# Performance work log

Hardware: AMD Instinct MI355X
Metric: run time of the kernel (lower is better)

The kernel has to match this reference:

```python
import jax, jax.numpy as jnp
import numpy as np

N_NODES = 100000
N_EDGES = 1600000
D = 128
NUM_EXPERTS = 8
NUM_LAYERS = 2
EPS = 1e-5


def setup_inputs() -> dict:
    key = jax.random.key(0)
    ks = jax.random.split(key, 8)
    x = jax.random.normal(ks[0], (N_NODES, D), dtype=jnp.float32)
    edge_index = jax.random.randint(ks[1], (2, N_EDGES), 0, N_NODES, dtype=jnp.int64)
    # weights scaled for sane numerics (like torch default inits)
    W_self = jax.random.normal(ks[2], (NUM_EXPERTS, NUM_LAYERS, D, D), dtype=jnp.float32) * 0.05
    W_nbr = jax.random.normal(ks[3], (NUM_EXPERTS, NUM_LAYERS, D, D), dtype=jnp.float32) * 0.05
    b = jax.random.normal(ks[4], (NUM_EXPERTS, NUM_LAYERS, D), dtype=jnp.float32) * 0.05
    gamma = jnp.ones((NUM_EXPERTS, NUM_LAYERS - 1, D), dtype=jnp.float32)
    beta = jnp.zeros((NUM_EXPERTS, NUM_LAYERS - 1, D), dtype=jnp.float32)
    return {"x": x, "edge_index": edge_index, "W_self": W_self, "W_nbr": W_nbr,
            "b": b, "gamma": gamma, "beta": beta}


def _sage_encoder(x, src, dst, inv_deg, W_self, W_nbr, b, gamma, beta):
    # One GraphSAGE-style encoder: per layer, mean-aggregate neighbor feats,
    # transform self + neighbor, then BatchNorm + ReLU (all but last layer).
    h = x
    for l in range(NUM_LAYERS):
        agg = jax.ops.segment_sum(h[src], dst, num_segments=N_NODES) * inv_deg  # [N, d]
        h = h @ W_self[l] + agg @ W_nbr[l] + b[l]
        if l < NUM_LAYERS - 1:
            mean = jnp.mean(h, axis=0)
            var = jnp.var(h, axis=0)
            h = gamma[l] * (h - mean) * jax.lax.rsqrt(var + EPS) + beta[l]
            h = jax.nn.relu(h)
        # dropout: identity in inference mode
    return h  # [N, d]


def reference(x, edge_index, W_self, W_nbr, b, gamma, beta):
    src, dst = edge_index[0], edge_index[1]
    deg = jax.ops.segment_sum(jnp.ones((N_EDGES,), x.dtype), dst, num_segments=N_NODES)
    inv_deg = (1.0 / jnp.maximum(deg, 1.0))[:, None]  # [N, 1]
    outs = [
        _sage_encoder(x, src, dst, inv_deg, W_self[e], W_nbr[e], b[e], gamma[e], beta[e])
        for e in range(NUM_EXPERTS)
    ]
    return jnp.stack(outs, axis=-1)  # [N, hidden, num_experts]
```

## Files before the change

### kernel.cpp

```cpp
#include <hip/hip_runtime.h>
#include <stdint.h>

#define NN 100000
#define NED 1600000
#define DD 128
#define NE 8
#define ND ((size_t)NN * (size_t)DD)
#define NDE (ND * NE)
#define BNEPS 1e-5f

typedef __attribute__((ext_vector_type(8))) short short8;
typedef __attribute__((ext_vector_type(4))) float float4v;
typedef __attribute__((ext_vector_type(4))) unsigned int uint4v;

__device__ __forceinline__ float bf2f(uint32_t h) {
    union { uint32_t u; float f; } c; c.u = h << 16; return c.f;
}
__device__ __forceinline__ uint16_t f2bf(float x) {
    union { float f; uint32_t u; } c; c.f = x;
    uint32_t r = (c.u + 0x7fffu + ((c.u >> 16) & 1u)) >> 16;
    return (uint16_t)r;
}

__global__ __launch_bounds__(256) void k_deg(const int* __restrict__ dst, int* __restrict__ deg) {
    int i = blockIdx.x * 256 + threadIdx.x;
    int stride = gridDim.x * 256;
    for (; i < NED; i += stride) atomicAdd(&deg[dst[i]], 1);
}

__global__ __launch_bounds__(1024) void k_scan1(const int* __restrict__ deg, int* __restrict__ rp,
                                                int* __restrict__ bsum) {
    __shared__ int sh[1024];
    int t = threadIdx.x;
    int i = blockIdx.x * 1024 + t;
    int v = (i < NN) ? deg[i] : 0;
    sh[t] = v; __syncthreads();
    for (int off = 1; off < 1024; off <<= 1) {
        int add = (t >= off) ? sh[t - off] : 0;
        __syncthreads();
        sh[t] += add;
        __syncthreads();
    }
    if (i < NN) rp[i] = sh[t] - v;
    if (t == 1023) bsum[blockIdx.x] = sh[1023];
}

__global__ void k_scan2(int* bsum) {
    if (threadIdx.x == 0) {
        int acc = 0;
        for (int j = 0; j < 98; ++j) { int t = bsum[j]; bsum[j] = acc; acc += t; }
    }
}

__global__ __launch_bounds__(1024) void k_scan3(const int* __restrict__ deg, int* __restrict__ rp,
                                                const int* __restrict__ bsum, int* __restrict__ cur,
                                                float* __restrict__ invd) {
    int i = blockIdx.x * 1024 + threadIdx.x;
    if (i == 0) rp[NN] = NED;
    if (i < NN) {
        int r = rp[i] + bsum[blockIdx.x];
        rp[i] = r; cur[i] = r;
        invd[i] = 1.0f / fmaxf((float)deg[i], 1.0f);
    }
}

__global__ __launch_bounds__(256) void k_scatter(const int* __restrict__ src, const int* __restrict__ dst,
                                                 int* __restrict__ cur, int* __restrict__ esrc) {
    int i = blockIdx.x * 256 + threadIdx.x;
    int stride = gridDim.x * 256;
    for (; i < NED; i += stride) {
        int d = dst[i];
        int p = atomicAdd(&cur[d], 1);
        esrc[p] = src[i];
    }
}

__global__ __launch_bounds__(256) void k_castx(const float* __restrict__ x, uint16_t* __restrict__ xb) {
    size_t i = ((size_t)blockIdx.x * 256 + threadIdx.x) * 8;
    if (i >= ND) return;
    float4 a = *(const float4*)(x + i);
    float4 b = *(const float4*)(x + i + 4);
    uint4 u;
    u.x = (uint32_t)f2bf(a.x) | ((uint32_t)f2bf(a.y) << 16);
    u.y = (uint32_t)f2bf(a.z) | ((uint32_t)f2bf(a.w) << 16);
    u.z = (uint32_t)f2bf(b.x) | ((uint32_t)f2bf(b.y) << 16);
    u.w = (uint32_t)f2bf(b.z) | ((uint32_t)f2bf(b.w) << 16);
    *(uint4*)(xb + i) = u;
}

__global__ __launch_bounds__(256) void k_agg(const uint16_t* __restrict__ sp, uint16_t* __restrict__ dp,
                                             const int* __restrict__ rp, const int* __restrict__ esrc,
                                             const float* __restrict__ invd) {
    int wave = threadIdx.x >> 6, lane = threadIdx.x & 63;
    int node = blockIdx.x * 4 + wave;
    if (node >= NN) return;
    int beg = rp[node], end = rp[node + 1];
    float s0 = 0, s1 = 0, t0 = 0, t1 = 0, u0 = 0, u1 = 0, w0 = 0, w1 = 0;
    int i = beg;
    for (; i + 3 < end; i += 4) {
        int a = esrc[i], b = esrc[i + 1], c = esrc[i + 2], d = esrc[i + 3];
        uint32_t va = *(const uint32_t*)(sp + (size_t)a * DD + lane * 2);
        uint32_t vb = *(const uint32_t*)(sp + (size_t)b * DD + lane * 2);
        uint32_t vc = *(const uint32_t*)(sp + (size_t)c * DD + lane * 2);
        uint32_t vd = *(const uint32_t*)(sp + (size_t)d * DD + lane * 2);
        s0 += bf2f(va & 0xffff); s1 += bf2f(va >> 16);
        t0 += bf2f(vb & 0xffff); t1 += bf2f(vb >> 16);
        u0 += bf2f(vc & 0xffff); u1 += bf2f(vc >> 16);
        w0 += bf2f(vd & 0xffff); w1 += bf2f(vd >> 16);
    }
    for (; i < end; ++i) {
        uint32_t va = *(const uint32_t*)(sp + (size_t)esrc[i] * DD + lane * 2);
        s0 += bf2f(va & 0xffff); s1 += bf2f(va >> 16);
    }
    float id = invd[node];
    s0 = (s0 + t0 + u0 + w0) * id; s1 = (s1 + t1 + u1 + w1) * id;
    *(uint32_t*)(dp + (size_t)node * DD + lane * 2) = (uint32_t)f2bf(s0) | ((uint32_t)f2bf(s1) << 16);
}

__device__ __forceinline__ void acc_u4(float* a, uint4 u) {
    a[0] += bf2f(u.x & 0xffffu); a[1] += bf2f(u.x >> 16);
    a[2] += bf2f(u.y & 0xffffu); a[3] += bf2f(u.y >> 16);
    a[4] += bf2f(u.z & 0xffffu); a[5] += bf2f(u.z >> 16);
    a[6] += bf2f(u.w & 0xffffu); a[7] += bf2f(u.w >> 16);
}

__global__ __launch_bounds__(256) void k_agg8(const uint16_t* __restrict__ Hi,
                                              uint16_t* __restrict__ A2i,
                                              const int* __restrict__ rp,
                                              const int* __restrict__ esrc,
                                              const float* __restrict__ invd) {
    int wave = threadIdx.x >> 6, lane = threadIdx.x & 63;
    int node = blockIdx.x * 4 + wave;
    if (node >= NN) return;
    int beg = rp[node], end = rp[node + 1];
    float acc[16];
#pragma unroll
    for (int j = 0; j < 16; ++j) acc[j] = 0.f;
    const size_t loff = (size_t)(lane * 16);
    int i = beg;
    for (; i + 3 < end; i += 4) {
        const uint16_t* p0 = Hi + (size_t)esrc[i] * 1024 + loff;
        const uint16_t* p1 = Hi + (size_t)esrc[i + 1] * 1024 + loff;
        const uint16_t* p2 = Hi + (size_t)esrc[i + 2] * 1024 + loff;
        const uint16_t* p3 = Hi + (size_t)esrc[i + 3] * 1024 + loff;
        uint4 a0 = *(const uint4*)p0;
        uint4 a1 = *(const uint4*)(p0 + 8);
        uint4 b0 = *(const uint4*)p1;
        uint4 b1 = *(const uint4*)(p1 + 8);
        uint4 c0 = *(const uint4*)p2;
        uint4 c1 = *(const uint4*)(p2 + 8);
        uint4 d0 = *(const uint4*)p3;
        uint4 d1 = *(const uint4*)(p3 + 8);
        acc_u4(acc, a0); acc_u4(acc + 8, a1);
        acc_u4(acc, b0); acc_u4(acc + 8, b1);
        acc_u4(acc, c0); acc_u4(acc + 8, c1);
        acc_u4(acc, d0); acc_u4(acc + 8, d1);
    }
    for (; i < end; ++i) {
        const uint16_t* pa = Hi + (size_t)esrc[i] * 1024 + loff;
        uint4 a0 = *(const uint4*)pa;
        uint4 a1 = *(const uint4*)(pa + 8);
        acc_u4(acc, a0); acc_u4(acc + 8, a1);
    }
    float id = invd[node];
    uint32_t pk[8];
#pragma unroll
    for (int j = 0; j < 8; ++j)
        pk[j] = (uint32_t)f2bf(acc[2 * j] * id) | ((uint32_t)f2bf(acc[2 * j + 1] * id) << 16);
    uint4v o0 = {pk[0], pk[1], pk[2], pk[3]};
    uint4v o1 = {pk[4], pk[5], pk[6], pk[7]};
    uint16_t* dp = A2i + (size_t)node * 1024 + loff;
    __builtin_nontemporal_store(o0, (uint4v*)dp);
    __builtin_nontemporal_store(o1, (uint4v*)(dp + 8));
}

__global__ __launch_bounds__(256, 2) void k_gemm(
    const float* __restrict__ Wself, const float* __restrict__ Wnbr, const float* __restrict__ bglob,
    int layer,
    const uint16_t* __restrict__ A1, const uint16_t* __restrict__ A2, int a_rstride, int a_ezoff,
    uint16_t* __restrict__ outb, int out_mode, float* __restrict__ outf,
    int do_stats, float* __restrict__ stats) {
    __shared__ __align__(16) uint16_t wlds[128 * 256];
    __shared__ float ssum[128];
    __shared__ float ssq[128];
    int tid = threadIdx.x;
    int e = blockIdx.z;
    size_t wbase = ((size_t)e * 2 + layer) * (128 * 128);

    for (int i = tid; i < 128 * 32; i += 256) {
        int n = i & 127, g = i >> 7;
        uint16_t tmp[8];
#pragma unroll
        for (int j = 0; j < 8; ++j) {
            int k = g * 8 + j;
            float w = (k < 128) ? Wself[wbase + (size_t)k * 128 + n]
                                : Wnbr[wbase + (size_t)(k - 128) * 128 + n];
            tmp[j] = f2bf(w);
        }
        uint4 u;
        u.x = (uint32_t)tmp[0] | ((uint32_t)tmp[1] << 16);
        u.y = (uint32_t)tmp[2] | ((uint32_t)tmp[3] << 16);
        u.z = (uint32_t)tmp[4] | ((uint32_t)tmp[5] << 16);
        u.w = (uint32_t)tmp[6] | ((uint32_t)tmp[7] << 16);
        *(uint4*)&wlds[n * 256 + (((g ^ n) & 31) << 3)] = u;
    }
    if (tid < 128) { ssum[tid] = 0.f; ssq[tid] = 0.f; }
    __syncthreads();

    const uint16_t* A1p = A1 + (size_t)e * a_ezoff;
    const uint16_t* A2p = A2 + (size_t)e * a_ezoff;

    int wave = tid >> 6, lane = tid & 63;
    int m = lane & 15, quad = lane >> 4;
    int rowBase = blockIdx.x * 256 + wave * 64;

    float4v acc[4][8];
#pragma unroll
    for (int rt = 0; rt < 4; ++rt)
#pragma unroll
        for (int nt = 0; nt < 8; ++nt)
            acc[rt][nt] = (float4v){0.f, 0.f, 0.f, 0.f};

#pragma unroll
    for (int ks = 0; ks < 8; ++ks) {
        int kk = ks * 32 + quad * 8;
        short8 af[4];
#pragma unroll
        for (int rt = 0; rt < 4; ++rt) {
            int row = rowBase + rt * 16 + m;
            row = row < NN ? row : NN - 1;
            const uint16_t* ap = (kk < 128) ? (A1p + (size_t)row * a_rstride + kk)
                                            : (A2p + (size_t)row * a_rstride + (kk - 128));
            af[rt] = *(const short8*)ap;
        }
        int g = kk >> 3;
#pragma unroll
        for (int nt = 0; nt < 8; ++nt) {
            int n = nt * 16 + m;
            short8 bf = *(const short8*)&wlds[n * 256 + (((g ^ n) & 31) << 3)];
#pragma unroll
            for (int rt = 0; rt < 4; ++rt)
                acc[rt][nt] = __builtin_amdgcn_mfma_f32_16x16x32_bf16(af[rt], bf, acc[rt][nt], 0, 0, 0);
        }
    }

    float csum[8], csq[8];
#pragma unroll
    for (int nt = 0; nt < 8; ++nt) { csum[nt] = 0.f; csq[nt] = 0.f; }

    size_t bofs = ((size_t)e * 2 + layer) * 128;
#pragma unroll
    for (int rt = 0; rt < 4; ++rt) {
#pragma unroll
        for (int nt = 0; nt < 8; ++nt) {
            int col = nt * 16 + m;
            float bv = bglob[bofs + col];
#pragma unroll
            for (int r = 0; r < 4; ++r) {
                int row = rowBase + rt * 16 + quad * 4 + r;
                if (row < NN) {
                    float v = acc[rt][nt][r] + bv;
                    if (out_mode == 0) outb[(size_t)row * 1024 + (size_t)e * 128 + col] = f2bf(v);
                    else if (out_mode == 1) outb[(size_t)e * ND + (size_t)row * DD + col] = f2bf(v);
                    else outf[(size_t)row * 1024 + col * 8 + e] = v;
                    if (do_stats) { csum[nt] += v; csq[nt] += v * v; }
                }
            }
        }
    }

    if (do_stats) {
#pragma unroll
        for (int nt = 0; nt < 8; ++nt) {
            float s = csum[nt], q = csq[nt];
            s += __shfl_xor(s, 16); q += __shfl_xor(q, 16);
            s += __shfl_xor(s, 32); q += __shfl_xor(q, 32);
            if (quad == 0) {
                atomicAdd(&ssum[nt * 16 + m], s);
                atomicAdd(&ssq[nt * 16 + m], q);
            }
        }
        __syncthreads();
        if (tid < 128) {
            atomicAdd(&stats[e * 256 + tid], ssum[tid]);
            atomicAdd(&stats[e * 256 + 128 + tid], ssq[tid]);
        }
    }
}

__global__ void k_coef(const float* __restrict__ stats, const float* __restrict__ gamma,
                       const float* __restrict__ beta, float* __restrict__ coef) {
    int e = blockIdx.x;
    int f = threadIdx.x;
    float s = stats[e * 256 + f], ss = stats[e * 256 + 128 + f];
    float mean = s / (float)NN;
    float var = ss / (float)NN - mean * mean;
    float sc = gamma[e * 128 + f] * rsqrtf(var + BNEPS);
    coef[e * 256 + f] = sc;
    coef[e * 256 + 128 + f] = beta[e * 128 + f] - mean * sc;
}

__global__ __launch_bounds__(256) void k_affine(uint16_t* __restrict__ H, const float* __restrict__ coef) {
    size_t i = ((size_t)blockIdx.x * 256 + threadIdx.x) * 8;
    if (i >= NDE) return;
    int e = (int)((i >> 7) & 7);
    int ff = (int)(i & 127);
    const float* sc = coef + e * 256;
    const float* sf = sc + 128;
    uint4 u = *(const uint4*)(H + i);
    uint32_t w[4] = {u.x, u.y, u.z, u.w};
    uint32_t o[4];
#pragma unroll
    for (int j = 0; j < 4; ++j) {
        float v0 = fmaxf(bf2f(w[j] & 0xffffu) * sc[ff + 2 * j] + sf[ff + 2 * j], 0.f);
        float v1 = fmaxf(bf2f(w[j] >> 16) * sc[ff + 2 * j + 1] + sf[ff + 2 * j + 1], 0.f);
        o[j] = (uint32_t)f2bf(v0) | ((uint32_t)f2bf(v1) << 16);
    }
    uint4 ou = {o[0], o[1], o[2], o[3]};
    *(uint4*)(H + i) = ou;
}

__global__ __launch_bounds__(256) void k_transpose(const uint16_t* __restrict__ O, float* __restrict__ out) {
    size_t t = (size_t)blockIdx.x * 256 + threadIdx.x;
    if (t >= ND / 2) return;
    size_t idx = t * 2;
    float v0[8], v1[8];
#pragma unroll
    for (int e = 0; e < 8; ++e) {
        uint32_t u = *(const uint32_t*)(O + (size_t)e * ND + idx);
        v0[e] = bf2f(u & 0xffff); v1[e] = bf2f(u >> 16);
    }
    float* op = out + idx * 8;
    float4 a = {v0[0], v0[1], v0[2], v0[3]}, b = {v0[4], v0[5], v0[6], v0[7]};
    float4 c = {v1[0], v1[1], v1[2], v1[3]}, d = {v1[4], v1[5], v1[6], v1[7]};
    *(float4*)(op) = a; *(float4*)(op + 4) = b; *(float4*)(op + 8) = c; *(float4*)(op + 12) = d;
}

extern "C" void kernel_launch(void* const* d_in, const int* in_sizes, int n_in,
                              void* d_out, int out_size, void* d_ws, size_t ws_size,
                              hipStream_t stream) {
    const float* x = (const float*)d_in[0];
    const int* ei = (const int*)d_in[1];
    const float* Wself = (const float*)d_in[2];
    const float* Wnbr = (const float*)d_in[3];
    const float* bias = (const float*)d_in[4];
    const float* gamma = (const float*)d_in[5];
    const float* beta = (const float*)d_in[6];
    float* out = (float*)d_out;
    const int* src = ei;
    const int* dst = ei + NED;

    char* ws = (char*)d_ws;
    size_t off = 0;
    auto alloc = [&](size_t b) { size_t p = off; off += (b + 255) & ~(size_t)255; return p; };
    int* deg = (int*)(ws + alloc((size_t)NN * 4));
    int* rp = (int*)(ws + alloc((size_t)(NN + 1) * 4));
    int* cur = (int*)(ws + alloc((size_t)NN * 4));
    int* esrc = (int*)(ws + alloc((size_t)NED * 4));
    float* invd = (float*)(ws + alloc((size_t)NN * 4));
    int* bsum = (int*)(ws + alloc(98 * 4));
    float* stats = (float*)(ws + alloc(NE * 256 * 4));
    float* coef = (float*)(ws + alloc(NE * 256 * 4));
    uint16_t* xb = (uint16_t*)(ws + alloc(ND * 2));
    uint16_t* agg0 = (uint16_t*)(ws + alloc(ND * 2));

    size_t rem = (ws_size > off) ? ws_size - off : 0;
    size_t plane = ND * 2;
    bool useO = rem >= 24 * plane + 4096;

    uint16_t* Hi = (uint16_t*)(ws + alloc(NE * plane));
    uint16_t* A2i = (uint16_t*)(ws + alloc(NE * plane));
    uint16_t* Otmp = useO ? (uint16_t*)(ws + alloc((size_t)NE * plane)) : nullptr;

    hipMemsetAsync(deg, 0, (size_t)NN * 4, stream);
    hipMemsetAsync(stats, 0, NE * 256 * 4, stream);

    k_deg<<<2048, 256, 0, stream>>>(dst, deg);
    k_scan1<<<98, 1024, 0, stream>>>(deg, rp, bsum);
    k_scan2<<<1, 64, 0, stream>>>(bsum);
    k_scan3<<<98, 1024, 0, stream>>>(deg, rp, bsum, cur, invd);
    k_scatter<<<2048, 256, 0, stream>>>(src, dst, cur, esrc);
    k_castx<<<6250, 256, 0, stream>>>(x, xb);

    k_agg<<<25000, 256, 0, stream>>>(xb, agg0, rp, esrc, invd);

    k_gemm<<<dim3(391, 1, NE), 256, 0, stream>>>(Wself, Wnbr, bias, 0,
                                                 xb, agg0, 128, 0, Hi, 0, nullptr, 1, stats);
    k_coef<<<NE, 128, 0, stream>>>(stats, gamma, beta, coef);
    k_affine<<<50000, 256, 0, stream>>>(Hi, coef);

    k_agg8<<<25000, 256, 0, stream>>>(Hi, A2i, rp, esrc, invd);

    if (useO) {
        k_gemm<<<dim3(391, 1, NE), 256, 0, stream>>>(Wself, Wnbr, bias, 1,
                                                     Hi, A2i, 1024, 128, Otmp, 1, nullptr, 0, nullptr);
        k_transpose<<<25000, 256, 0, stream>>>(Otmp, out);
    } else {
        k_gemm<<<dim3(391, 1, NE), 256, 0, stream>>>(Wself, Wnbr, bias, 1,
                                                     Hi, A2i, 1024, 128, nullptr, 2, out, 0, nullptr);
    }
}
```

Baseline: 1.928 ms.

## Coalesce edge-index loads via shuffles and split agg8 rows across two waves

Both aggregation kernels now load up to 64 edge source indices at once, one per lane, and broadcast them with __shfl. This replaces the earlier pattern where every lane redundantly read the same esrc entries, and lets each wave issue eight independent gathers per iteration. k_agg8 now gives each node two waves, one per half of the 1024-element row. That halves per-lane accumulator registers and doubles the number of blocks launched, at the cost of each wave reading the node's edge list separately. The transpose output writes become nontemporal stores.

New measurement: 2.242 ms. +16.2%, slower.

```diff
diff --git a/kernel.cpp b/kernel.cpp
--- a/kernel.cpp
+++ b/kernel.cpp
@@ -95,25 +95,37 @@
     int node = blockIdx.x * 4 + wave;
     if (node >= NN) return;
     int beg = rp[node], end = rp[node + 1];
-    float s0 = 0, s1 = 0, t0 = 0, t1 = 0, u0 = 0, u1 = 0, w0 = 0, w1 = 0;
-    int i = beg;
-    for (; i + 3 < end; i += 4) {
-        int a = esrc[i], b = esrc[i + 1], c = esrc[i + 2], d = esrc[i + 3];
-        uint32_t va = *(const uint32_t*)(sp + (size_t)a * DD + lane * 2);
-        uint32_t vb = *(const uint32_t*)(sp + (size_t)b * DD + lane * 2);
-        uint32_t vc = *(const uint32_t*)(sp + (size_t)c * DD + lane * 2);
-        uint32_t vd = *(const uint32_t*)(sp + (size_t)d * DD + lane * 2);
-        s0 += bf2f(va & 0xffff); s1 += bf2f(va >> 16);
-        t0 += bf2f(vb & 0xffff); t1 += bf2f(vb >> 16);
-        u0 += bf2f(vc & 0xffff); u1 += bf2f(vc >> 16);
-        w0 += bf2f(vd & 0xffff); w1 += bf2f(vd >> 16);
-    }
-    for (; i < end; ++i) {
-        uint32_t va = *(const uint32_t*)(sp + (size_t)esrc[i] * DD + lane * 2);
-        s0 += bf2f(va & 0xffff); s1 += bf2f(va >> 16);
+    float s0 = 0, s1 = 0, t0 = 0, t1 = 0;
+    const uint16_t* Hb = sp + (size_t)lane * 2;
+    for (int base = beg; base < end; base += 64) {
+        int cnt = end - base; if (cnt > 64) cnt = 64;
+        int myidx = (lane < cnt) ? esrc[base + lane] : 0;
+        int j = 0;
+        for (; j + 8 <= cnt; j += 8) {
+            uint32_t v0 = *(const uint32_t*)(Hb + (size_t)__shfl(myidx, j + 0) * DD);
+            uint32_t v1 = *(const uint32_t*)(Hb + (size_t)__shfl(myidx, j + 1) * DD);
+            uint32_t v2 = *(const uint32_t*)(Hb + (size_t)__shfl(myidx, j + 2) * DD);
+            uint32_t v3 = *(const uint32_t*)(Hb + (size_t)__shfl(myidx, j + 3) * DD);
+            uint32_t v4 = *(const uint32_t*)(Hb + (size_t)__shfl(myidx, j + 4) * DD);
+            uint32_t v5 = *(const uint32_t*)(Hb + (size_t)__shfl(myidx, j + 5) * DD);
+            uint32_t v6 = *(const uint32_t*)(Hb + (size_t)__shfl(myidx, j + 6) * DD);
+            uint32_t v7 = *(const uint32_t*)(Hb + (size_t)__shfl(myidx, j + 7) * DD);
+            s0 += bf2f(v0 & 0xffff); s1 += bf2f(v0 >> 16);
+            t0 += bf2f(v1 & 0xffff); t1 += bf2f(v1 >> 16);
+            s0 += bf2f(v2 & 0xffff); s1 += bf2f(v2 >> 16);
+            t0 += bf2f(v3 & 0xffff); t1 += bf2f(v3 >> 16);
+            s0 += bf2f(v4 & 0xffff); s1 += bf2f(v4 >> 16);
+            t0 += bf2f(v5 & 0xffff); t1 += bf2f(v5 >> 16);
+            s0 += bf2f(v6 & 0xffff); s1 += bf2f(v6 >> 16);
+            t0 += bf2f(v7 & 0xffff); t1 += bf2f(v7 >> 16);
+        }
+        for (; j < cnt; ++j) {
+            uint32_t v = *(const uint32_t*)(Hb + (size_t)__shfl(myidx, j) * DD);
+            s0 += bf2f(v & 0xffff); s1 += bf2f(v >> 16);
+        }
     }
     float id = invd[node];
-    s0 = (s0 + t0 + u0 + w0) * id; s1 = (s1 + t1 + u1 + w1) * id;
+    s0 = (s0 + t0) * id; s1 = (s1 + t1) * id;
     *(uint32_t*)(dp + (size_t)node * DD + lane * 2) = (uint32_t)f2bf(s0) | ((uint32_t)f2bf(s1) << 16);
 }
 
@@ -129,49 +141,46 @@
                                               const int* __restrict__ rp,
                                               const int* __restrict__ esrc,
                                               const float* __restrict__ invd) {
-    int wave = threadIdx.x >> 6, lane = threadIdx.x & 63;
-    int node = blockIdx.x * 4 + wave;
+    int wid = blockIdx.x * 4 + (threadIdx.x >> 6);
+    int node = wid >> 1;
     if (node >= NN) return;
+    int half = wid & 1, lane = threadIdx.x & 63;
     int beg = rp[node], end = rp[node + 1];
-    float acc[16];
-#pragma unroll
-    for (int j = 0; j < 16; ++j) acc[j] = 0.f;
-    const size_t loff = (size_t)(lane * 16);
-    int i = beg;
-    for (; i + 3 < end; i += 4) {
-        const uint16_t* p0 = Hi + (size_t)esrc[i] * 1024 + loff;
-        const uint16_t* p1 = Hi + (size_t)esrc[i + 1] * 1024 + loff;
-        const uint16_t* p2 = Hi + (size_t)esrc[i + 2] * 1024 + loff;
-        const uint16_t* p3 = Hi + (size_t)esrc[i + 3] * 1024 + loff;
-        uint4 a0 = *(const uint4*)p0;
-        uint4 a1 = *(const uint4*)(p0 + 8);
-        uint4 b0 = *(const uint4*)p1;
-        uint4 b1 = *(const uint4*)(p1 + 8);
-        uint4 c0 = *(const uint4*)p2;
-        uint4 c1 = *(const uint4*)(p2 + 8);
-        uint4 d0 = *(const uint4*)p3;
-        uint4 d1 = *(const uint4*)(p3 + 8);
-        acc_u4(acc, a0); acc_u4(acc + 8, a1);
-        acc_u4(acc, b0); acc_u4(acc + 8, b1);
-        acc_u4(acc, c0); acc_u4(acc + 8, c1);
-        acc_u4(acc, d0); acc_u4(acc + 8, d1);
-    }
-    for (; i < end; ++i) {
-        const uint16_t* pa = Hi + (size_t)esrc[i] * 1024 + loff;
-        uint4 a0 = *(const uint4*)pa;
-        uint4 a1 = *(const uint4*)(pa + 8);
-        acc_u4(acc, a0); acc_u4(acc + 8, a1);
+    float acc[8];
+#pragma unroll
+    for (int j = 0; j < 8; ++j) acc[j] = 0.f;
+    const uint16_t* Hb = Hi + (size_t)half * 512 + (size_t)lane * 8;
+    for (int base = beg; base < end; base += 64) {
+        int cnt = end - base; if (cnt > 64) cnt = 64;
+        int myidx = (lane < cnt) ? esrc[base + lane] : 0;
+        int j = 0;
+        for (; j + 8 <= cnt; j += 8) {
+            uint4 v0 = *(const uint4*)(Hb + (size_t)__shfl(myidx, j + 0) * 1024);
+            uint4 v1 = *(const uint4*)(Hb + (size_t)__shfl(myidx, j + 1) * 1024);
+            uint4 v2 = *(const uint4*)(Hb + (size_t)__shfl(myidx, j + 2) * 1024);
+            uint4 v3 = *(const uint4*)(Hb + (size_t)__shfl(myidx, j + 3) * 1024);
+            uint4 v4 = *(const uint4*)(Hb + (size_t)__shfl(myidx, j + 4) * 1024);
+            uint4 v5 = *(const uint4*)(Hb + (size_t)__shfl(myidx, j + 5) * 1024);
+            uint4 v6 = *(const uint4*)(Hb + (size_t)__shfl(myidx, j + 6) * 1024);
+            uint4 v7 = *(const uint4*)(Hb + (size_t)__shfl(myidx, j + 7) * 1024);
+            acc_u4(acc, v0); acc_u4(acc, v1);
+            acc_u4(acc, v2); acc_u4(acc, v3);
+            acc_u4(acc, v4); acc_u4(acc, v5);
+            acc_u4(acc, v6); acc_u4(acc, v7);
+        }
+        for (; j < cnt; ++j) {
+            uint4 v = *(const uint4*)(Hb + (size_t)__shfl(myidx, j) * 1024);
+            acc_u4(acc, v);
+        }
     }
     float id = invd[node];
-    uint32_t pk[8];
-#pragma unroll
-    for (int j = 0; j < 8; ++j)
+    uint32_t pk[4];
+#pragma unroll
+    for (int j = 0; j < 4; ++j)
         pk[j] = (uint32_t)f2bf(acc[2 * j] * id) | ((uint32_t)f2bf(acc[2 * j + 1] * id) << 16);
-    uint4v o0 = {pk[0], pk[1], pk[2], pk[3]};
-    uint4v o1 = {pk[4], pk[5], pk[6], pk[7]};
-    uint16_t* dp = A2i + (size_t)node * 1024 + loff;
-    __builtin_nontemporal_store(o0, (uint4v*)dp);
-    __builtin_nontemporal_store(o1, (uint4v*)(dp + 8));
+    uint4v o = {pk[0], pk[1], pk[2], pk[3]};
+    uint16_t* dp = A2i + (size_t)node * 1024 + (size_t)half * 512 + (size_t)lane * 8;
+    __builtin_nontemporal_store(o, (uint4v*)dp);
 }
 
 __global__ __launch_bounds__(256, 2) void k_gemm(
@@ -331,9 +340,12 @@
         v0[e] = bf2f(u & 0xffff); v1[e] = bf2f(u >> 16);
     }
     float* op = out + idx * 8;
-    float4 a = {v0[0], v0[1], v0[2], v0[3]}, b = {v0[4], v0[5], v0[6], v0[7]};
-    float4 c = {v1[0], v1[1], v1[2], v1[3]}, d = {v1[4], v1[5], v1[6], v1[7]};
-    *(float4*)(op) = a; *(float4*)(op + 4) = b; *(float4*)(op + 8) = c; *(float4*)(op + 12) = d;
+    float4v a = {v0[0], v0[1], v0[2], v0[3]}, b = {v0[4], v0[5], v0[6], v0[7]};
+    float4v c = {v1[0], v1[1], v1[2], v1[3]}, d = {v1[4], v1[5], v1[6], v1[7]};
+    __builtin_nontemporal_store(a, (float4v*)(op));
+    __builtin_nontemporal_store(b, (float4v*)(op + 4));
+    __builtin_nontemporal_store(c, (float4v*)(op + 8));
+    __builtin_nontemporal_store(d, (float4v*)(op + 12));
 }
 
 extern "C" void kernel_launch(void* const* d_in, const int* in_sizes, int n_in,
@@ -389,7 +401,7 @@
     k_coef<<<NE, 128, 0, stream>>>(stats, gamma, beta, coef);
     k_affine<<<50000, 256, 0, stream>>>(Hi, coef);
 
-    k_agg8<<<25000, 256, 0, stream>>>(Hi, A2i, rp, esrc, invd);
+    k_agg8<<<50000, 256, 0, stream>>>(Hi, A2i, rp, esrc, invd);
 
     if (useO) {
         k_gemm<<<dim3(391, 1, NE), 256, 0, stream>>>(Wself, Wnbr, bias, 1,
```
